# Kernel optimization log

Measured on AMD Instinct MI355X. Metric: run time of the kernel, lower is better.

The kernel has to match this reference:

```python
import jax, jax.numpy as jnp
import numpy as np

N = 20000; E = 320000; F_IN = 128; H = 4; D = 32; HD = 128; G = 8; C = 10


def _ln(x, g, b):
    mu = x.mean(-1, keepdims=True)
    v = ((x - mu) ** 2).mean(-1, keepdims=True)
    return (x - mu) / jnp.sqrt(v + 1e-5) * g + b


def _tconv(x, src, dst, attr, Wq, Wk, Wv, We, Ws, bq, bk, bv, be, bs):
    # PyG TransformerConv (concat=True, beta=False, root_weight=True), eval mode
    n = x.shape[0]
    q = (x @ Wq + bq).reshape(n, H, D)[dst]            # [E,H,D] gather at targets i
    k = (x @ Wk + bk).reshape(n, H, D)[src]            # [E,H,D] gather at sources j
    v = (x @ Wv + bv).reshape(n, H, D)[src]
    ef = (attr @ We + be).reshape(-1, H, D)            # edge features lifted to [E,H,D]
    k = k + ef
    v = v + ef
    logit = (q * k).sum(-1) / jnp.sqrt(jnp.float32(D))  # [E,H]
    m = jax.ops.segment_max(logit, dst, num_segments=n)
    m = jnp.where(jnp.isfinite(m), m, 0.0)
    ex = jnp.exp(logit - m[dst])
    s = jax.ops.segment_sum(ex, dst, num_segments=n)
    alpha = ex / (s[dst] + 1e-16)                      # segment softmax over incoming edges
    out = jax.ops.segment_sum(v * alpha[..., None], dst, num_segments=n).reshape(n, HD)
    out = out + x @ Ws + bs                            # skip / root weight
    return out, alpha


def setup_inputs() -> dict:
    key = jax.random.key(0)
    ks = jax.random.split(key, 50)
    inp = {}
    inp["x"] = jax.random.normal(ks[0], (N, F_IN), jnp.float32)
    inp["edge_index"] = jax.random.randint(ks[1], (2, E), 0, N)
    inp["attr"] = jax.random.normal(ks[2], (E, 1), jnp.float32)
    inp["batch"] = jnp.sort(jax.random.randint(ks[3], (N,), 0, G))
    i = 4
    for l, din in zip((1, 2, 3), (F_IN, HD, HD)):
        for nm, shp in (("Wq", (din, HD)), ("Wk", (din, HD)), ("Wv", (din, HD)), ("We", (1, HD)), ("Ws", (din, HD))):
            inp[f"{nm}{l}"] = jax.random.normal(ks[i], shp, jnp.float32) * 0.05
            i += 1
        for nm in ("bq", "bk", "bv", "be", "bs"):
            inp[f"{nm}{l}"] = jnp.zeros((HD,), jnp.float32)
    inp["ln1_g"] = jnp.ones((HD,), jnp.float32); inp["ln1_b"] = jnp.zeros((HD,), jnp.float32)
    inp["ln2_g"] = jnp.ones((HD,), jnp.float32); inp["ln2_b"] = jnp.zeros((HD,), jnp.float32)
    inp["fc1_w"] = jax.random.normal(ks[i], (HD, HD), jnp.float32) * 0.05; i += 1
    inp["fc1_b"] = jnp.zeros((HD,), jnp.float32)
    inp["cln_g"] = jnp.ones((HD,), jnp.float32); inp["cln_b"] = jnp.zeros((HD,), jnp.float32)
    inp["fc2_w"] = jax.random.normal(ks[i], (HD, C), jnp.float32) * 0.05
    inp["fc2_b"] = jnp.zeros((C,), jnp.float32)
    return inp


def reference(x, edge_index, attr, batch,
              Wq1, Wk1, Wv1, We1, Ws1, bq1, bk1, bv1, be1, bs1,
              Wq2, Wk2, Wv2, We2, Ws2, bq2, bk2, bv2, be2, bs2,
              Wq3, Wk3, Wv3, We3, Ws3, bq3, bk3, bv3, be3, bs3,
              ln1_g, ln1_b, ln2_g, ln2_b,
              fc1_w, fc1_b, cln_g, cln_b, fc2_w, fc2_b):
    src, dst = edge_index[0], edge_index[1]
    h, a1 = _tconv(x, src, dst, attr, Wq1, Wk1, Wv1, We1, Ws1, bq1, bk1, bv1, be1, bs1)
    h = jax.nn.relu(_ln(h, ln1_g, ln1_b))              # dropout is identity in eval
    h, a2 = _tconv(h, src, dst, attr, Wq2, Wk2, Wv2, We2, Ws2, bq2, bk2, bv2, be2, bs2)
    h = jax.nn.relu(_ln(h, ln2_g, ln2_b))
    z, a3 = _tconv(h, src, dst, attr, Wq3, Wk3, Wv3, We3, Ws3, bq3, bk3, bv3, be3, bs3)
    # global mean pool over graphs
    cnt = jax.ops.segment_sum(jnp.ones((N,), z.dtype), batch, num_segments=G)
    z_pool = jax.ops.segment_sum(z, batch, num_segments=G) / jnp.maximum(cnt, 1.0)[:, None]
    # classifier
    hcl = jax.nn.relu(_ln(z_pool @ fc1_w + fc1_b, cln_g, cln_b))
    probs = jax.nn.softmax(hcl @ fc2_w + fc2_b, axis=1)
    z_sel = z_pool[batch[0]]
    return (z, z_sel, probs, a1, a2, a3)
```

## Files before the change

kernel.cpp:

```cpp
#include <hip/hip_runtime.h>


typedef short short8v __attribute__((ext_vector_type(8)));
typedef float f32x4 __attribute__((ext_vector_type(4)));

__device__ __forceinline__ unsigned pack_bf16_rne(float a, float b) {
    unsigned ua = __float_as_uint(a);
    ua += 0x7fffu + ((ua >> 16) & 1u);
    unsigned ub = __float_as_uint(b);
    ub += 0x7fffu + ((ub >> 16) & 1u);
    return (ua >> 16) | (ub & 0xffff0000u);
}

__device__ __forceinline__ unsigned short bf16_rne1(float a) {
    unsigned u = __float_as_uint(a);
    u += 0x7fffu + ((u >> 16) & 1u);
    return (unsigned short)(u >> 16);
}

__global__ __launch_bounds__(256) void hist_kernel(const int* __restrict__ dst,
                                                   int* __restrict__ cnt, int E) {
    int e = blockIdx.x * 256 + threadIdx.x;
    if (e < E) atomicAdd(&cnt[dst[e]], 1);
}

__global__ __launch_bounds__(1024) void scan_kernel(const int* __restrict__ cnt,
                                                    int* __restrict__ rowptr, int n) {
    __shared__ int wls[16];
    __shared__ int carry;
    const int tid = threadIdx.x, lane = tid & 63, wid = tid >> 6;
    if (tid == 0) { carry = 0; rowptr[0] = 0; }
    __syncthreads();
    for (int base = 0; base < n; base += 1024) {
        int i = base + tid;
        int v = (i < n) ? cnt[i] : 0;
        int sc = v;
        for (int off = 1; off < 64; off <<= 1) {
            int t = __shfl_up(sc, off);
            if (lane >= off) sc += t;
        }
        if (lane == 63) wls[wid] = sc;
        __syncthreads();
        if (tid == 0) {
            int run = carry;
            for (int w2 = 0; w2 < 16; ++w2) { int t = wls[w2]; wls[w2] = run; run += t; }
            carry = run;
        }
        __syncthreads();
        if (i < n) rowptr[i + 1] = wls[wid] + sc;
        __syncthreads();
    }
}

__global__ __launch_bounds__(256) void fill_kernel(const int* __restrict__ src,
                                                   const int* __restrict__ dst,
                                                   const float* __restrict__ attr,
                                                   const int* __restrict__ rowptr,
                                                   int* __restrict__ tmp,
                                                   int* __restrict__ src_perm,
                                                   float* __restrict__ attr_perm,
                                                   int* __restrict__ eidp, int E) {
    int e = blockIdx.x * 256 + threadIdx.x;
    if (e < E) {
        int d = dst[e];
        int p = atomicAdd(&tmp[d], 1);
        int pos = rowptr[d] + p;
        src_perm[pos] = src[e];
        attr_perm[pos] = attr[e];
        eidp[pos] = e;
    }
}

__global__ __launch_bounds__(256) void cvt_bf16_kernel(const float* __restrict__ in,
                                                       unsigned* __restrict__ outp, int n32) {
    int i = blockIdx.x * 256 + threadIdx.x;
    if (i < n32) {
        float2 v = *(const float2*)&in[(size_t)i * 2];
        outp[i] = pack_bf16_rne(v.x, v.y);
    }
}

__global__ __launch_bounds__(256) void prepack_kernel(
    const float* __restrict__ W0, const float* __restrict__ W1,
    const float* __restrict__ W2, const float* __restrict__ W3,
    unsigned* __restrict__ wt) {
    const int m = blockIdx.y;
    const float* W = (m == 0) ? W0 : (m == 1) ? W1 : (m == 2) ? W2 : W3;
    int idx = blockIdx.x * 256 + threadIdx.x;
    int c = idx >> 6;
    int kp = idx & 63;
    float w0 = W[(size_t)(2 * kp) * 128 + c];
    float w1 = W[(size_t)(2 * kp + 1) * 128 + c];
    wt[(size_t)m * 8192 + (size_t)c * 64 + kp] = pack_bf16_rne(w0, w1);
}

__global__ __launch_bounds__(256) void gemm_mfma_kernel(
    const unsigned short* __restrict__ Xb, const unsigned short* __restrict__ wt,
    const float* __restrict__ bq, const float* __restrict__ bk,
    const float* __restrict__ bv, const float* __restrict__ bs,
    float* __restrict__ qo, unsigned short* __restrict__ ko,
    unsigned short* __restrict__ vo, float* __restrict__ so, int nrows) {
    const int lane = threadIdx.x & 63;
    const int w = threadIdx.x >> 6;
    const int m = blockIdx.y;
    const int strip = blockIdx.x * 64 + w * 16;
    const int arow = strip + (lane & 15);
    const int arow_c = min(arow, nrows - 1);
    const int kblk = (lane >> 4) * 8;
    const unsigned short* Wm = wt + (size_t)m * 16384;
    const float* bias = (m == 0) ? bq : (m == 1) ? bk : (m == 2) ? bv : bs;

    f32x4 acc[8];
#pragma unroll
    for (int f = 0; f < 8; ++f) acc[f] = (f32x4){0.f, 0.f, 0.f, 0.f};

#pragma unroll
    for (int ks = 0; ks < 4; ++ks) {
        const int k0 = ks * 32 + kblk;
        const short8v a = *(const short8v*)&Xb[(size_t)arow_c * 128 + k0];
#pragma unroll
        for (int f = 0; f < 8; ++f) {
            const short8v b = *(const short8v*)&Wm[(size_t)(f * 16 + (lane & 15)) * 128 + k0];
            acc[f] = __builtin_amdgcn_mfma_f32_16x16x32_bf16(a, b, acc[f], 0, 0, 0);
        }
    }

    const int r0 = strip + (lane >> 4) * 4;
#pragma unroll
    for (int f = 0; f < 8; ++f) {
        const int col = f * 16 + (lane & 15);
        const float bv_ = bias[col];
        if (m == 0 || m == 3) {
            float* OUT = (m == 0) ? qo : so;
#pragma unroll
            for (int r = 0; r < 4; ++r) {
                int row = r0 + r;
                if (row < nrows) OUT[(size_t)row * 128 + col] = acc[f][r] + bv_;
            }
        } else {
            unsigned short* OUT = (m == 1) ? ko : vo;
#pragma unroll
            for (int r = 0; r < 4; ++r) {
                int row = r0 + r;
                if (row < nrows) OUT[(size_t)row * 128 + col] = bf16_rne1(acc[f][r] + bv_);
            }
        }
    }
}

__global__ __launch_bounds__(256) void node_fused_kernel(
    const float* __restrict__ qb, const unsigned* __restrict__ kb,
    const unsigned* __restrict__ vb,
    const float* __restrict__ Wev, const float* __restrict__ bev,
    const int* __restrict__ rowptr, const int* __restrict__ src_perm,
    const float* __restrict__ attr_perm, const int* __restrict__ eidp,
    float* __restrict__ alpha_perm, float* __restrict__ alpha_out,
    float* __restrict__ out, int n) {
    __shared__ float alds[4][64][4];
    const int wid = threadIdx.x >> 6;
    const int node = blockIdx.x * 4 + wid;
    const int lane = threadIdx.x & 63;
    if (node >= n) return;
    const int start = rowptr[node], end = rowptr[node + 1];
    const int deg = end - start;
    if (deg == 0) return;

    const float we0 = Wev[2 * lane], we1 = Wev[2 * lane + 1];
    const float be0 = bev[2 * lane], be1 = bev[2 * lane + 1];
    const float2 qv = *(const float2*)&qb[(size_t)node * 128 + 2 * lane];
    const float scale = 0.17677669529663687f;
    const int h = lane >> 4;

    if (deg <= 64) {
        const bool valid = lane < deg;
        const int j = start + lane;
        const int sj = valid ? src_perm[j] : 0;
        const float aj = valid ? attr_perm[j] : 0.f;

        int t = 0;
        for (; t + 1 < deg; t += 2) {
            const int s0 = __shfl(sj, t), s1 = __shfl(sj, t + 1);
            const float a0 = __shfl(aj, t), a1 = __shfl(aj, t + 1);
            const unsigned u0 = kb[(size_t)s0 * 64 + lane];
            const unsigned u1 = kb[(size_t)s1 * 64 + lane];
            float p0 = qv.x * (__uint_as_float(u0 << 16) + a0 * we0 + be0)
                     + qv.y * (__uint_as_float(u0 & 0xffff0000u) + a0 * we1 + be1);
            float p1 = qv.x * (__uint_as_float(u1 << 16) + a1 * we0 + be0)
                     + qv.y * (__uint_as_float(u1 & 0xffff0000u) + a1 * we1 + be1);
#pragma unroll
            for (int off = 1; off < 16; off <<= 1) {
                p0 += __shfl_xor(p0, off);
                p1 += __shfl_xor(p1, off);
            }
            if ((lane & 15) == 0) {
                alds[wid][t][h] = p0 * scale;
                alds[wid][t + 1][h] = p1 * scale;
            }
        }
        if (t < deg) {
            const int s0 = __shfl(sj, t);
            const float a0 = __shfl(aj, t);
            const unsigned u0 = kb[(size_t)s0 * 64 + lane];
            float p0 = qv.x * (__uint_as_float(u0 << 16) + a0 * we0 + be0)
                     + qv.y * (__uint_as_float(u0 & 0xffff0000u) + a0 * we1 + be1);
#pragma unroll
            for (int off = 1; off < 16; off <<= 1) p0 += __shfl_xor(p0, off);
            if ((lane & 15) == 0) alds[wid][t][h] = p0 * scale;
        }

        float4 lg = valid ? *(const float4*)&alds[wid][lane][0]
                          : make_float4(-1e30f, -1e30f, -1e30f, -1e30f);
        float4 mx = lg;
#pragma unroll
        for (int off = 1; off < 64; off <<= 1) {
            mx.x = fmaxf(mx.x, __shfl_xor(mx.x, off));
            mx.y = fmaxf(mx.y, __shfl_xor(mx.y, off));
            mx.z = fmaxf(mx.z, __shfl_xor(mx.z, off));
            mx.w = fmaxf(mx.w, __shfl_xor(mx.w, off));
        }
        float4 ev;
        ev.x = __expf(lg.x - mx.x); ev.y = __expf(lg.y - mx.y);
        ev.z = __expf(lg.z - mx.z); ev.w = __expf(lg.w - mx.w);
        float4 s4 = ev;
#pragma unroll
        for (int off = 1; off < 64; off <<= 1) {
            s4.x += __shfl_xor(s4.x, off); s4.y += __shfl_xor(s4.y, off);
            s4.z += __shfl_xor(s4.z, off); s4.w += __shfl_xor(s4.w, off);
        }
        float4 al;
        al.x = ev.x / (s4.x + 1e-16f); al.y = ev.y / (s4.y + 1e-16f);
        al.z = ev.z / (s4.z + 1e-16f); al.w = ev.w / (s4.w + 1e-16f);
        if (valid) *(float4*)&alpha_out[(size_t)eidp[j] * 4] = al;
        *(float4*)&alds[wid][lane][0] = al;

        float acc0 = 0.f, acc1 = 0.f;
        t = 0;
        for (; t + 1 < deg; t += 2) {
            const int s0 = __shfl(sj, t), s1 = __shfl(sj, t + 1);
            const float a0 = __shfl(aj, t), a1 = __shfl(aj, t + 1);
            const float w0 = alds[wid][t][h];
            const float w1 = alds[wid][t + 1][h];
            const unsigned u0 = vb[(size_t)s0 * 64 + lane];
            const unsigned u1 = vb[(size_t)s1 * 64 + lane];
            acc0 += w0 * (__uint_as_float(u0 << 16) + a0 * we0 + be0)
                  + w1 * (__uint_as_float(u1 << 16) + a1 * we0 + be0);
            acc1 += w0 * (__uint_as_float(u0 & 0xffff0000u) + a0 * we1 + be1)
                  + w1 * (__uint_as_float(u1 & 0xffff0000u) + a1 * we1 + be1);
        }
        if (t < deg) {
            const int s0 = __shfl(sj, t);
            const float a0 = __shfl(aj, t);
            const float w0 = alds[wid][t][h];
            const unsigned u0 = vb[(size_t)s0 * 64 + lane];
            acc0 += w0 * (__uint_as_float(u0 << 16) + a0 * we0 + be0);
            acc1 += w0 * (__uint_as_float(u0 & 0xffff0000u) + a0 * we1 + be1);
        }
        float2 o = *(float2*)&out[(size_t)node * 128 + 2 * lane];
        o.x += acc0; o.y += acc1;
        *(float2*)&out[(size_t)node * 128 + 2 * lane] = o;
        return;
    }

    float mh = -1e30f;
    for (int c0 = start; c0 < end; c0 += 64) {
        const int nc = min(64, end - c0);
        const int sj = (lane < nc) ? src_perm[c0 + lane] : 0;
        const float aj = (lane < nc) ? attr_perm[c0 + lane] : 0.f;
        int t = 0;
        for (; t + 1 < nc; t += 2) {
            const int s0 = __shfl(sj, t), s1 = __shfl(sj, t + 1);
            const float a0 = __shfl(aj, t), a1 = __shfl(aj, t + 1);
            const unsigned u0 = kb[(size_t)s0 * 64 + lane];
            const unsigned u1 = kb[(size_t)s1 * 64 + lane];
            float p0 = qv.x * (__uint_as_float(u0 << 16) + a0 * we0 + be0)
                     + qv.y * (__uint_as_float(u0 & 0xffff0000u) + a0 * we1 + be1);
            float p1 = qv.x * (__uint_as_float(u1 << 16) + a1 * we0 + be0)
                     + qv.y * (__uint_as_float(u1 & 0xffff0000u) + a1 * we1 + be1);
#pragma unroll
            for (int off = 1; off < 16; off <<= 1) {
                p0 += __shfl_xor(p0, off);
                p1 += __shfl_xor(p1, off);
            }
            p0 *= scale; p1 *= scale;
            mh = fmaxf(mh, fmaxf(p0, p1));
            if ((lane & 15) == 0) {
                alpha_perm[(size_t)(c0 + t) * 4 + h] = p0;
                alpha_perm[(size_t)(c0 + t + 1) * 4 + h] = p1;
            }
        }
        if (t < nc) {
            const int s0 = __shfl(sj, t);
            const float a0 = __shfl(aj, t);
            const unsigned u0 = kb[(size_t)s0 * 64 + lane];
            float p0 = qv.x * (__uint_as_float(u0 << 16) + a0 * we0 + be0)
                     + qv.y * (__uint_as_float(u0 & 0xffff0000u) + a0 * we1 + be1);
#pragma unroll
            for (int off = 1; off < 16; off <<= 1) p0 += __shfl_xor(p0, off);
            p0 *= scale;
            mh = fmaxf(mh, p0);
            if ((lane & 15) == 0) alpha_perm[(size_t)(c0 + t) * 4 + h] = p0;
        }
    }
    const float m0 = __shfl(mh, 0), m1 = __shfl(mh, 16);
    const float m2 = __shfl(mh, 32), m3 = __shfl(mh, 48);

    float4 s4 = make_float4(0.f, 0.f, 0.f, 0.f);
    for (int c0 = start; c0 < end; c0 += 64) {
        const int j = c0 + lane;
        if (j < end) {
            float4 lg = *(const float4*)&alpha_perm[(size_t)j * 4];
            lg.x = __expf(lg.x - m0); lg.y = __expf(lg.y - m1);
            lg.z = __expf(lg.z - m2); lg.w = __expf(lg.w - m3);
            *(float4*)&alpha_perm[(size_t)j * 4] = lg;
            s4.x += lg.x; s4.y += lg.y; s4.z += lg.z; s4.w += lg.w;
        }
    }
#pragma unroll
    for (int off = 1; off < 64; off <<= 1) {
        s4.x += __shfl_xor(s4.x, off); s4.y += __shfl_xor(s4.y, off);
        s4.z += __shfl_xor(s4.z, off); s4.w += __shfl_xor(s4.w, off);
    }
    const float i0 = 1.f / (s4.x + 1e-16f), i1 = 1.f / (s4.y + 1e-16f);
    const float i2 = 1.f / (s4.z + 1e-16f), i3 = 1.f / (s4.w + 1e-16f);

    float acc0 = 0.f, acc1 = 0.f;
    for (int c0 = start; c0 < end; c0 += 64) {
        const int nc = min(64, end - c0);
        const int j = c0 + lane;
        if (lane < nc) {
            float4 ex = *(const float4*)&alpha_perm[(size_t)j * 4];
            float4 al;
            al.x = ex.x * i0; al.y = ex.y * i1; al.z = ex.z * i2; al.w = ex.w * i3;
            *(float4*)&alpha_out[(size_t)eidp[j] * 4] = al;
            *(float4*)&alds[wid][lane][0] = al;
        }
        const int sj = (lane < nc) ? src_perm[j] : 0;
        const float aj = (lane < nc) ? attr_perm[j] : 0.f;
        int t = 0;
        for (; t + 1 < nc; t += 2) {
            const int s0 = __shfl(sj, t), s1 = __shfl(sj, t + 1);
            const float a0 = __shfl(aj, t), a1 = __shfl(aj, t + 1);
            const float w0 = alds[wid][t][h];
            const float w1 = alds[wid][t + 1][h];
            const unsigned u0 = vb[(size_t)s0 * 64 + lane];
            const unsigned u1 = vb[(size_t)s1 * 64 + lane];
            acc0 += w0 * (__uint_as_float(u0 << 16) + a0 * we0 + be0)
                  + w1 * (__uint_as_float(u1 << 16) + a1 * we0 + be0);
            acc1 += w0 * (__uint_as_float(u0 & 0xffff0000u) + a0 * we1 + be1)
                  + w1 * (__uint_as_float(u1 & 0xffff0000u) + a1 * we1 + be1);
        }
        if (t < nc) {
            const int s0 = __shfl(sj, t);
            const float a0 = __shfl(aj, t);
            const float w0 = alds[wid][t][h];
            const unsigned u0 = vb[(size_t)s0 * 64 + lane];
            acc0 += w0 * (__uint_as_float(u0 << 16) + a0 * we0 + be0);
            acc1 += w0 * (__uint_as_float(u0 & 0xffff0000u) + a0 * we1 + be1);
        }
    }
    float2 o = *(float2*)&out[(size_t)node * 128 + 2 * lane];
    o.x += acc0; o.y += acc1;
    *(float2*)&out[(size_t)node * 128 + 2 * lane] = o;
}

__global__ __launch_bounds__(256) void ln_relu_kernel(const float* __restrict__ hin,
                                                      unsigned* __restrict__ hb,
                                                      const float* __restrict__ g,
                                                      const float* __restrict__ b, int n) {
    const int row = (blockIdx.x * 256 + threadIdx.x) >> 6;
    const int lane = threadIdx.x & 63;
    if (row >= n) return;
    const float2 xv = *(const float2*)&hin[(size_t)row * 128 + 2 * lane];
    float s = xv.x + xv.y;
#pragma unroll
    for (int off = 1; off < 64; off <<= 1) s += __shfl_xor(s, off);
    const float mu = s * (1.f / 128.f);
    const float d0 = xv.x - mu, d1 = xv.y - mu;
    float vs = d0 * d0 + d1 * d1;
#pragma unroll
    for (int off = 1; off < 64; off <<= 1) vs += __shfl_xor(vs, off);
    const float inv = rsqrtf(vs * (1.f / 128.f) + 1e-5f);
    const float2 gv = *(const float2*)&g[2 * lane];
    const float2 bv = *(const float2*)&b[2 * lane];
    const float n0 = fmaxf(d0 * inv * gv.x + bv.x, 0.f);
    const float n1 = fmaxf(d1 * inv * gv.y + bv.y, 0.f);
    hb[(size_t)row * 64 + lane] = pack_bf16_rne(n0, n1);
}

__global__ __launch_bounds__(128) void pool_kernel(const float* __restrict__ z,
                                                   const int* __restrict__ batch,
                                                   float* __restrict__ pool,
                                                   int* __restrict__ gcnt, int n) {
    const int c = threadIdx.x;
    const int row0 = blockIdx.x * 32;
    if (row0 >= n) return;
    const int rend = min(row0 + 32, n);
    int cur = batch[row0];
    float acc = 0.f;
    int run = 0;
    for (int r = row0; r < rend; ++r) {
        const int g = batch[r];
        if (g != cur) {
            atomicAdd(&pool[cur * 128 + c], acc);
            if (c == 0) atomicAdd(&gcnt[cur], run);
            acc = 0.f; run = 0; cur = g;
        }
        acc += z[(size_t)r * 128 + c];
        ++run;
    }
    atomicAdd(&pool[cur * 128 + c], acc);
    if (c == 0) atomicAdd(&gcnt[cur], run);
}

__global__ __launch_bounds__(128) void classifier_kernel(
    const float* __restrict__ pool, const int* __restrict__ gcnt,
    const int* __restrict__ batch,
    const float* __restrict__ fc1_w, const float* __restrict__ fc1_b,
    const float* __restrict__ cg, const float* __restrict__ cbv,
    const float* __restrict__ fc2_w, const float* __restrict__ fc2_b,
    float* __restrict__ zsel, float* __restrict__ probs) {
    __shared__ float zp[8][128];
    __shared__ float hc[8][128];
    __shared__ float red[2];
    __shared__ float lgt[8][10];
    const int c = threadIdx.x;
    const int lane = c & 63, wid = c >> 6;
#pragma unroll
    for (int g = 0; g < 8; ++g)
        zp[g][c] = pool[g * 128 + c] / fmaxf((float)gcnt[g], 1.f);
    __syncthreads();
    zsel[c] = zp[batch[0]][c];

    float acc[8];
#pragma unroll
    for (int g = 0; g < 8; ++g) acc[g] = fc1_b[c];
    for (int k = 0; k < 128; ++k) {
        const float w = fc1_w[k * 128 + c];
#pragma unroll
        for (int g = 0; g < 8; ++g) acc[g] += zp[g][k] * w;
    }
#pragma unroll
    for (int g = 0; g < 8; ++g) {
        float s = acc[g];
        for (int off = 1; off < 64; off <<= 1) s += __shfl_xor(s, off);
        if (lane == 0) red[wid] = s;
        __syncthreads();
        const float mu = (red[0] + red[1]) * (1.f / 128.f);
        __syncthreads();
        const float d = acc[g] - mu;
        float s2 = d * d;
        for (int off = 1; off < 64; off <<= 1) s2 += __shfl_xor(s2, off);
        if (lane == 0) red[wid] = s2;
        __syncthreads();
        const float var = (red[0] + red[1]) * (1.f / 128.f);
        __syncthreads();
        hc[g][c] = fmaxf(d * rsqrtf(var + 1e-5f) * cg[c] + cbv[c], 0.f);
    }
    __syncthreads();
    if (c < 80) {
        const int g = c / 10, j = c - g * 10;
        float s = fc2_b[j];
        for (int k = 0; k < 128; ++k) s += hc[g][k] * fc2_w[k * 10 + j];
        lgt[g][j] = s;
    }
    __syncthreads();
    if (c < 8) {
        float mx = -1e30f;
#pragma unroll
        for (int j = 0; j < 10; ++j) mx = fmaxf(mx, lgt[c][j]);
        float ex[10];
        float sum = 0.f;
#pragma unroll
        for (int j = 0; j < 10; ++j) { ex[j] = expf(lgt[c][j] - mx); sum += ex[j]; }
#pragma unroll
        for (int j = 0; j < 10; ++j) probs[c * 10 + j] = ex[j] / sum;
    }
}


extern "C" void kernel_launch(void* const* d_in, const int* in_sizes, int n_in,
                              void* d_out, int out_size, void* d_ws, size_t ws_size,
                              hipStream_t stream) {
    const float* x = (const float*)d_in[0];
    const int* edge_index = (const int*)d_in[1];
    const float* attr = (const float*)d_in[2];
    const int* batch = (const int*)d_in[3];
    const int N = in_sizes[0] / 128;
    const int E = in_sizes[2];
    const int* src = edge_index;
    const int* dst = edge_index + E;

    const float *Wq[3], *Wk[3], *Wv[3], *We[3], *Ws[3];
    const float *bq[3], *bk[3], *bv[3], *be[3], *bs[3];
    int idx = 4;
    for (int l = 0; l < 3; ++l) {
        Wq[l] = (const float*)d_in[idx++];
        Wk[l] = (const float*)d_in[idx++];
        Wv[l] = (const float*)d_in[idx++];
        We[l] = (const float*)d_in[idx++];
        Ws[l] = (const float*)d_in[idx++];
        bq[l] = (const float*)d_in[idx++];
        bk[l] = (const float*)d_in[idx++];
        bv[l] = (const float*)d_in[idx++];
        be[l] = (const float*)d_in[idx++];
        bs[l] = (const float*)d_in[idx++];
    }
    const float* ln_g[2] = {(const float*)d_in[34], (const float*)d_in[36]};
    const float* ln_b[2] = {(const float*)d_in[35], (const float*)d_in[37]};
    const float* fc1_w = (const float*)d_in[38];
    const float* fc1_b = (const float*)d_in[39];
    const float* cln_g = (const float*)d_in[40];
    const float* cln_b = (const float*)d_in[41];
    const float* fc2_w = (const float*)d_in[42];
    const float* fc2_b = (const float*)d_in[43];
    const int C = in_sizes[43];

    float* out = (float*)d_out;
    float* z_out = out;
    float* zsel_out = out + (size_t)N * 128;
    float* probs_out = zsel_out + 128;
    const int GC = out_size - N * 128 - 128 - 3 * E * 4;
    const int G = GC / C;
    float* alpha_out[3];
    alpha_out[0] = probs_out + GC;
    alpha_out[1] = alpha_out[0] + (size_t)E * 4;
    alpha_out[2] = alpha_out[1] + (size_t)E * 4;

    char* p = (char*)d_ws;
    auto alloc = [&](size_t bytes) {
        void* r = (void*)p;
        p += (bytes + 255) & ~(size_t)255;
        return r;
    };
    float* qb = (float*)alloc((size_t)N * 128 * 4);
    unsigned* kb = (unsigned*)alloc((size_t)N * 64 * 4);
    unsigned* vb = (unsigned*)alloc((size_t)N * 64 * 4);
    float* hA = (float*)alloc((size_t)N * 128 * 4);
    float* hB = (float*)alloc((size_t)N * 128 * 4);
    unsigned* xb = (unsigned*)alloc((size_t)N * 64 * 4);
    unsigned* hb = (unsigned*)alloc((size_t)N * 64 * 4);
    unsigned* wt = (unsigned*)alloc((size_t)12 * 8192 * 4);
    int* counts = (int*)alloc((size_t)N * 4);
    int* rowptr = (int*)alloc((size_t)(N + 1) * 4);
    int* cnt2 = (int*)alloc((size_t)N * 4);
    int* src_perm = (int*)alloc((size_t)E * 4);
    float* attr_perm = (float*)alloc((size_t)E * 4);
    int* eidp = (int*)alloc((size_t)E * 4);
    float* alpha_perm = (float*)alloc((size_t)E * 4 * 4);
    float* pool = (float*)alloc((size_t)G * 128 * 4);
    int* gcnt = (int*)alloc((size_t)G * 4);

    hipMemsetAsync(counts, 0, (size_t)N * 4, stream);
    hipMemsetAsync(cnt2, 0, (size_t)N * 4, stream);
    hipMemsetAsync(pool, 0, (size_t)G * 128 * 4, stream);
    hipMemsetAsync(gcnt, 0, (size_t)G * 4, stream);

    hist_kernel<<<(E + 255) / 256, 256, 0, stream>>>(dst, counts, E);
    scan_kernel<<<1, 1024, 0, stream>>>(counts, rowptr, N);
    fill_kernel<<<(E + 255) / 256, 256, 0, stream>>>(src, dst, attr, rowptr, cnt2,
                                                     src_perm, attr_perm, eidp, E);

    cvt_bf16_kernel<<<(N * 64 + 255) / 256, 256, 0, stream>>>(x, xb, N * 64);
    for (int l = 0; l < 3; ++l)
        prepack_kernel<<<dim3(32, 4), 256, 0, stream>>>(Wq[l], Wk[l], Wv[l], Ws[l],
                                                        wt + (size_t)l * 4 * 8192);

    for (int l = 0; l < 3; ++l) {
        float* OUTl = (l == 0) ? hA : (l == 1) ? hB : z_out;
        const unsigned short* Xin = (const unsigned short*)((l == 0) ? xb : hb);
        gemm_mfma_kernel<<<dim3((N + 63) / 64, 4), 256, 0, stream>>>(
            Xin, (const unsigned short*)(wt + (size_t)l * 4 * 8192),
            bq[l], bk[l], bv[l], bs[l],
            qb, (unsigned short*)kb, (unsigned short*)vb, OUTl, N);
        node_fused_kernel<<<(N + 3) / 4, 256, 0, stream>>>(
            qb, kb, vb, We[l], be[l], rowptr, src_perm, attr_perm, eidp,
            alpha_perm, alpha_out[l], OUTl, N);
        if (l < 2)
            ln_relu_kernel<<<((N + 3) / 4), 256, 0, stream>>>(OUTl, hb, ln_g[l], ln_b[l], N);
    }

    pool_kernel<<<(N + 31) / 32, 128, 0, stream>>>(z_out, batch, pool, gcnt, N);
    classifier_kernel<<<1, 128, 0, stream>>>(pool, gcnt, batch, fc1_w, fc1_b,
                                             cln_g, cln_b, fc2_w, fc2_b,
                                             zsel_out, probs_out);
}
```

Before: 523.9 us.

## Fuse LayerNorm+ReLU into node kernel, parallelize CSR scan, hoist edge-feature algebra

Folds the LayerNorm+ReLU epilogue into the per-node attention kernel, so the intermediate hidden state is never written and reread, which also removes two launches. The edge-feature terms are hoisted algebraically: q·we and q·be are reduced once per node, and the attention-weighted attr sum is applied once at the end. Both gather loops are unrolled by four for more memory-level parallelism. The single-block serial scan becomes a three-kernel parallel scan, and the three weight-prepack launches are merged into one. Costs are more register pressure in the fused kernel and slightly different float rounding order.

```diff
diff --git a/kernel.cpp b/kernel.cpp
--- a/kernel.cpp
+++ b/kernel.cpp
@@ -18,38 +18,67 @@
     return (unsigned short)(u >> 16);
 }
 
+__device__ __forceinline__ float blo(unsigned u) { return __uint_as_float(u << 16); }
+__device__ __forceinline__ float bhi(unsigned u) { return __uint_as_float(u & 0xffff0000u); }
+
 __global__ __launch_bounds__(256) void hist_kernel(const int* __restrict__ dst,
                                                    int* __restrict__ cnt, int E) {
     int e = blockIdx.x * 256 + threadIdx.x;
     if (e < E) atomicAdd(&cnt[dst[e]], 1);
 }
 
-__global__ __launch_bounds__(1024) void scan_kernel(const int* __restrict__ cnt,
-                                                    int* __restrict__ rowptr, int n) {
+__global__ __launch_bounds__(256) void blk_reduce_kernel(const int* __restrict__ cnt,
+                                                         int* __restrict__ bsum, int n) {
+    __shared__ int ws[4];
+    const int i = blockIdx.x * 256 + threadIdx.x;
+    const int lane = threadIdx.x & 63, wid = threadIdx.x >> 6;
+    int v = (i < n) ? cnt[i] : 0;
+#pragma unroll
+    for (int off = 1; off < 64; off <<= 1) v += __shfl_xor(v, off);
+    if (lane == 0) ws[wid] = v;
+    __syncthreads();
+    if (threadIdx.x == 0) bsum[blockIdx.x] = ws[0] + ws[1] + ws[2] + ws[3];
+}
+
+__global__ __launch_bounds__(1024) void blk_scan_kernel(int* __restrict__ bsum, int nb) {
     __shared__ int wls[16];
-    __shared__ int carry;
     const int tid = threadIdx.x, lane = tid & 63, wid = tid >> 6;
-    if (tid == 0) { carry = 0; rowptr[0] = 0; }
+    int v = (tid < nb) ? bsum[tid] : 0;
+    int sc = v;
+#pragma unroll
+    for (int off = 1; off < 64; off <<= 1) {
+        int t = __shfl_up(sc, off);
+        if (lane >= off) sc += t;
+    }
+    if (lane == 63) wls[wid] = sc;
     __syncthreads();
-    for (int base = 0; base < n; base += 1024) {
-        int i = base + tid;
-        int v = (i < n) ? cnt[i] : 0;
-        int sc = v;
-        for (int off = 1; off < 64; off <<= 1) {
-            int t = __shfl_up(sc, off);
-            if (lane >= off) sc += t;
-        }
-        if (lane == 63) wls[wid] = sc;
-        __syncthreads();
-        if (tid == 0) {
-            int run = carry;
-            for (int w2 = 0; w2 < 16; ++w2) { int t = wls[w2]; wls[w2] = run; run += t; }
-            carry = run;
-        }
-        __syncthreads();
-        if (i < n) rowptr[i + 1] = wls[wid] + sc;
-        __syncthreads();
-    }
+    if (tid == 0) {
+        int run = 0;
+        for (int w = 0; w < 16; ++w) { int t = wls[w]; wls[w] = run; run += t; }
+    }
+    __syncthreads();
+    if (tid < nb) bsum[tid] = wls[wid] + sc - v;
+}
+
+__global__ __launch_bounds__(256) void rowptr_fill_kernel(const int* __restrict__ cnt,
+                                                          const int* __restrict__ boff,
+                                                          int* __restrict__ rowptr, int n) {
+    __shared__ int wls[4];
+    const int i = blockIdx.x * 256 + threadIdx.x;
+    const int lane = threadIdx.x & 63, wid = threadIdx.x >> 6;
+    int v = (i < n) ? cnt[i] : 0;
+    int sc = v;
+#pragma unroll
+    for (int off = 1; off < 64; off <<= 1) {
+        int t = __shfl_up(sc, off);
+        if (lane >= off) sc += t;
+    }
+    if (lane == 63) wls[wid] = sc;
+    __syncthreads();
+    int add = boff[blockIdx.x];
+    for (int w = 0; w < wid; ++w) add += wls[w];
+    if (i < n) rowptr[i + 1] = sc + add;
+    if (i == 0) rowptr[0] = 0;
 }
 
 __global__ __launch_bounds__(256) void fill_kernel(const int* __restrict__ src,
@@ -80,18 +109,15 @@
     }
 }
 
-__global__ __launch_bounds__(256) void prepack_kernel(
-    const float* __restrict__ W0, const float* __restrict__ W1,
-    const float* __restrict__ W2, const float* __restrict__ W3,
-    unsigned* __restrict__ wt) {
+struct W12 { const float* p[12]; };
+__global__ __launch_bounds__(256) void prepack_all_kernel(W12 ws, unsigned* __restrict__ wt) {
     const int m = blockIdx.y;
-    const float* W = (m == 0) ? W0 : (m == 1) ? W1 : (m == 2) ? W2 : W3;
+    const float* W = ws.p[m];
     int idx = blockIdx.x * 256 + threadIdx.x;
     int c = idx >> 6;
     int kp = idx & 63;
-    float w0 = W[(size_t)(2 * kp) * 128 + c];
-    float w1 = W[(size_t)(2 * kp + 1) * 128 + c];
-    wt[(size_t)m * 8192 + (size_t)c * 64 + kp] = pack_bf16_rne(w0, w1);
+    wt[(size_t)m * 8192 + (size_t)c * 64 + kp] =
+        pack_bf16_rne(W[(size_t)(2 * kp) * 128 + c], W[(size_t)(2 * kp + 1) * 128 + c]);
 }
 
 __global__ __launch_bounds__(256) void gemm_mfma_kernel(
@@ -155,7 +181,10 @@
     const int* __restrict__ rowptr, const int* __restrict__ src_perm,
     const float* __restrict__ attr_perm, const int* __restrict__ eidp,
     float* __restrict__ alpha_perm, float* __restrict__ alpha_out,
-    float* __restrict__ out, int n) {
+    const float* __restrict__ skip, float* __restrict__ zout,
+    unsigned* __restrict__ hbout,
+    const float* __restrict__ lng, const float* __restrict__ lnb,
+    int do_ln, int n) {
     __shared__ float alds[4][64][4];
     const int wid = threadIdx.x >> 6;
     const int node = blockIdx.x * 4 + wid;
@@ -163,49 +192,63 @@
     if (node >= n) return;
     const int start = rowptr[node], end = rowptr[node + 1];
     const int deg = end - start;
-    if (deg == 0) return;
-
+    const int h = lane >> 4;
     const float we0 = Wev[2 * lane], we1 = Wev[2 * lane + 1];
     const float be0 = bev[2 * lane], be1 = bev[2 * lane + 1];
     const float2 qv = *(const float2*)&qb[(size_t)node * 128 + 2 * lane];
     const float scale = 0.17677669529663687f;
-    const int h = lane >> 4;
-
-    if (deg <= 64) {
+    const bool fastp = (deg <= 64);
+
+    float acc0 = 0.f, acc1 = 0.f, sa = 0.f;
+
+    if (deg > 0 && fastp) {
+        float pw = qv.x * we0 + qv.y * we1;
+        float pb = qv.x * be0 + qv.y * be1;
+#pragma unroll
+        for (int off = 1; off < 16; off <<= 1) {
+            pw += __shfl_xor(pw, off);
+            pb += __shfl_xor(pb, off);
+        }
+
         const bool valid = lane < deg;
         const int j = start + lane;
         const int sj = valid ? src_perm[j] : 0;
         const float aj = valid ? attr_perm[j] : 0.f;
 
         int t = 0;
-        for (; t + 1 < deg; t += 2) {
+        for (; t + 3 < deg; t += 4) {
             const int s0 = __shfl(sj, t), s1 = __shfl(sj, t + 1);
+            const int s2 = __shfl(sj, t + 2), s3 = __shfl(sj, t + 3);
             const float a0 = __shfl(aj, t), a1 = __shfl(aj, t + 1);
+            const float a2 = __shfl(aj, t + 2), a3 = __shfl(aj, t + 3);
             const unsigned u0 = kb[(size_t)s0 * 64 + lane];
             const unsigned u1 = kb[(size_t)s1 * 64 + lane];
-            float p0 = qv.x * (__uint_as_float(u0 << 16) + a0 * we0 + be0)
-                     + qv.y * (__uint_as_float(u0 & 0xffff0000u) + a0 * we1 + be1);
-            float p1 = qv.x * (__uint_as_float(u1 << 16) + a1 * we0 + be0)
-                     + qv.y * (__uint_as_float(u1 & 0xffff0000u) + a1 * we1 + be1);
+            const unsigned u2 = kb[(size_t)s2 * 64 + lane];
+            const unsigned u3 = kb[(size_t)s3 * 64 + lane];
+            float p0 = qv.x * blo(u0) + qv.y * bhi(u0);
+            float p1 = qv.x * blo(u1) + qv.y * bhi(u1);
+            float p2 = qv.x * blo(u2) + qv.y * bhi(u2);
+            float p3 = qv.x * blo(u3) + qv.y * bhi(u3);
 #pragma unroll
             for (int off = 1; off < 16; off <<= 1) {
-                p0 += __shfl_xor(p0, off);
-                p1 += __shfl_xor(p1, off);
+                p0 += __shfl_xor(p0, off); p1 += __shfl_xor(p1, off);
+                p2 += __shfl_xor(p2, off); p3 += __shfl_xor(p3, off);
             }
             if ((lane & 15) == 0) {
-                alds[wid][t][h] = p0 * scale;
-                alds[wid][t + 1][h] = p1 * scale;
-            }
-        }
-        if (t < deg) {
+                alds[wid][t + 0][h] = (p0 + a0 * pw + pb) * scale;
+                alds[wid][t + 1][h] = (p1 + a1 * pw + pb) * scale;
+                alds[wid][t + 2][h] = (p2 + a2 * pw + pb) * scale;
+                alds[wid][t + 3][h] = (p3 + a3 * pw + pb) * scale;
+            }
+        }
+        for (; t < deg; ++t) {
             const int s0 = __shfl(sj, t);
             const float a0 = __shfl(aj, t);
             const unsigned u0 = kb[(size_t)s0 * 64 + lane];
-            float p0 = qv.x * (__uint_as_float(u0 << 16) + a0 * we0 + be0)
-                     + qv.y * (__uint_as_float(u0 & 0xffff0000u) + a0 * we1 + be1);
+            float p0 = qv.x * blo(u0) + qv.y * bhi(u0);
 #pragma unroll
             for (int off = 1; off < 16; off <<= 1) p0 += __shfl_xor(p0, off);
-            if ((lane & 15) == 0) alds[wid][t][h] = p0 * scale;
+            if ((lane & 15) == 0) alds[wid][t][h] = (p0 + a0 * pw + pb) * scale;
         }
 
         float4 lg = valid ? *(const float4*)&alds[wid][lane][0]
@@ -233,158 +276,155 @@
         if (valid) *(float4*)&alpha_out[(size_t)eidp[j] * 4] = al;
         *(float4*)&alds[wid][lane][0] = al;
 
-        float acc0 = 0.f, acc1 = 0.f;
         t = 0;
-        for (; t + 1 < deg; t += 2) {
+        for (; t + 3 < deg; t += 4) {
             const int s0 = __shfl(sj, t), s1 = __shfl(sj, t + 1);
+            const int s2 = __shfl(sj, t + 2), s3 = __shfl(sj, t + 3);
             const float a0 = __shfl(aj, t), a1 = __shfl(aj, t + 1);
-            const float w0 = alds[wid][t][h];
+            const float a2 = __shfl(aj, t + 2), a3 = __shfl(aj, t + 3);
+            const float w0 = alds[wid][t + 0][h];
             const float w1 = alds[wid][t + 1][h];
+            const float w2 = alds[wid][t + 2][h];
+            const float w3 = alds[wid][t + 3][h];
             const unsigned u0 = vb[(size_t)s0 * 64 + lane];
             const unsigned u1 = vb[(size_t)s1 * 64 + lane];
-            acc0 += w0 * (__uint_as_float(u0 << 16) + a0 * we0 + be0)
-                  + w1 * (__uint_as_float(u1 << 16) + a1 * we0 + be0);
-            acc1 += w0 * (__uint_as_float(u0 & 0xffff0000u) + a0 * we1 + be1)
-                  + w1 * (__uint_as_float(u1 & 0xffff0000u) + a1 * we1 + be1);
-        }
-        if (t < deg) {
+            const unsigned u2 = vb[(size_t)s2 * 64 + lane];
+            const unsigned u3 = vb[(size_t)s3 * 64 + lane];
+            acc0 += w0 * blo(u0) + w1 * blo(u1) + w2 * blo(u2) + w3 * blo(u3);
+            acc1 += w0 * bhi(u0) + w1 * bhi(u1) + w2 * bhi(u2) + w3 * bhi(u3);
+            sa += w0 * a0 + w1 * a1 + w2 * a2 + w3 * a3;
+        }
+        for (; t < deg; ++t) {
             const int s0 = __shfl(sj, t);
             const float a0 = __shfl(aj, t);
             const float w0 = alds[wid][t][h];
             const unsigned u0 = vb[(size_t)s0 * 64 + lane];
-            acc0 += w0 * (__uint_as_float(u0 << 16) + a0 * we0 + be0);
-            acc1 += w0 * (__uint_as_float(u0 & 0xffff0000u) + a0 * we1 + be1);
-        }
-        float2 o = *(float2*)&out[(size_t)node * 128 + 2 * lane];
-        o.x += acc0; o.y += acc1;
-        *(float2*)&out[(size_t)node * 128 + 2 * lane] = o;
-        return;
-    }
-
-    float mh = -1e30f;
-    for (int c0 = start; c0 < end; c0 += 64) {
-        const int nc = min(64, end - c0);
-        const int sj = (lane < nc) ? src_perm[c0 + lane] : 0;
-        const float aj = (lane < nc) ? attr_perm[c0 + lane] : 0.f;
-        int t = 0;
-        for (; t + 1 < nc; t += 2) {
-            const int s0 = __shfl(sj, t), s1 = __shfl(sj, t + 1);
-            const float a0 = __shfl(aj, t), a1 = __shfl(aj, t + 1);
-            const unsigned u0 = kb[(size_t)s0 * 64 + lane];
-            const unsigned u1 = kb[(size_t)s1 * 64 + lane];
-            float p0 = qv.x * (__uint_as_float(u0 << 16) + a0 * we0 + be0)
-                     + qv.y * (__uint_as_float(u0 & 0xffff0000u) + a0 * we1 + be1);
-            float p1 = qv.x * (__uint_as_float(u1 << 16) + a1 * we0 + be0)
-                     + qv.y * (__uint_as_float(u1 & 0xffff0000u) + a1 * we1 + be1);
-#pragma unroll
-            for (int off = 1; off < 16; off <<= 1) {
-                p0 += __shfl_xor(p0, off);
-                p1 += __shfl_xor(p1, off);
-            }
-            p0 *= scale; p1 *= scale;
-            mh = fmaxf(mh, fmaxf(p0, p1));
-            if ((lane & 15) == 0) {
-                alpha_perm[(size_t)(c0 + t) * 4 + h] = p0;
-                alpha_perm[(size_t)(c0 + t + 1) * 4 + h] = p1;
-            }
-        }
-        if (t < nc) {
-            const int s0 = __shfl(sj, t);
-            const float a0 = __shfl(aj, t);
-            const unsigned u0 = kb[(size_t)s0 * 64 + lane];
-            float p0 = qv.x * (__uint_as_float(u0 << 16) + a0 * we0 + be0)
-                     + qv.y * (__uint_as_float(u0 & 0xffff0000u) + a0 * we1 + be1);
-#pragma unroll
-            for (int off = 1; off < 16; off <<= 1) p0 += __shfl_xor(p0, off);
-            p0 *= scale;
-            mh = fmaxf(mh, p0);
-            if ((lane & 15) == 0) alpha_perm[(size_t)(c0 + t) * 4 + h] = p0;
-        }
-    }
-    const float m0 = __shfl(mh, 0), m1 = __shfl(mh, 16);
-    const float m2 = __shfl(mh, 32), m3 = __shfl(mh, 48);
-
-    float4 s4 = make_float4(0.f, 0.f, 0.f, 0.f);
-    for (int c0 = start; c0 < end; c0 += 64) {
-        const int j = c0 + lane;
-        if (j < end) {
-            float4 lg = *(const float4*)&alpha_perm[(size_t)j * 4];
-            lg.x = __expf(lg.x - m0); lg.y = __expf(lg.y - m1);
-            lg.z = __expf(lg.z - m2); lg.w = __expf(lg.w - m3);
-            *(float4*)&alpha_perm[(size_t)j * 4] = lg;
-            s4.x += lg.x; s4.y += lg.y; s4.z += lg.z; s4.w += lg.w;
-        }
-    }
-#pragma unroll
-    for (int off = 1; off < 64; off <<= 1) {
-        s4.x += __shfl_xor(s4.x, off); s4.y += __shfl_xor(s4.y, off);
-        s4.z += __shfl_xor(s4.z, off); s4.w += __shfl_xor(s4.w, off);
-    }
-    const float i0 = 1.f / (s4.x + 1e-16f), i1 = 1.f / (s4.y + 1e-16f);
-    const float i2 = 1.f / (s4.z + 1e-16f), i3 = 1.f / (s4.w + 1e-16f);
-
-    float acc0 = 0.f, acc1 = 0.f;
-    for (int c0 = start; c0 < end; c0 += 64) {
-        const int nc = min(64, end - c0);
-        const int j = c0 + lane;
-        if (lane < nc) {
-            float4 ex = *(const float4*)&alpha_perm[(size_t)j * 4];
-            float4 al;
-            al.x = ex.x * i0; al.y = ex.y * i1; al.z = ex.z * i2; al.w = ex.w * i3;
-            *(float4*)&alpha_out[(size_t)eidp[j] * 4] = al;
-            *(float4*)&alds[wid][lane][0] = al;
-        }
-        const int sj = (lane < nc) ? src_perm[j] : 0;
-        const float aj = (lane < nc) ? attr_perm[j] : 0.f;
-        int t = 0;
-        for (; t + 1 < nc; t += 2) {
-            const int s0 = __shfl(sj, t), s1 = __shfl(sj, t + 1);
-            const float a0 = __shfl(aj, t), a1 = __shfl(aj, t + 1);
-            const float w0 = alds[wid][t][h];
-            const float w1 = alds[wid][t + 1][h];
-            const unsigned u0 = vb[(size_t)s0 * 64 + lane];
-            const unsigned u1 = vb[(size_t)s1 * 64 + lane];
-            acc0 += w0 * (__uint_as_float(u0 << 16) + a0 * we0 + be0)
-                  + w1 * (__uint_as_float(u1 << 16) + a1 * we0 + be0);
-            acc1 += w0 * (__uint_as_float(u0 & 0xffff0000u) + a0 * we1 + be1)
-                  + w1 * (__uint_as_float(u1 & 0xffff0000u) + a1 * we1 + be1);
-        }
-        if (t < nc) {
-            const int s0 = __shfl(sj, t);
-            const float a0 = __shfl(aj, t);
-            const float w0 = alds[wid][t][h];
-            const unsigned u0 = vb[(size_t)s0 * 64 + lane];
-            acc0 += w0 * (__uint_as_float(u0 << 16) + a0 * we0 + be0);
-            acc1 += w0 * (__uint_as_float(u0 & 0xffff0000u) + a0 * we1 + be1);
-        }
-    }
-    float2 o = *(float2*)&out[(size_t)node * 128 + 2 * lane];
-    o.x += acc0; o.y += acc1;
-    *(float2*)&out[(size_t)node * 128 + 2 * lane] = o;
-}
-
-__global__ __launch_bounds__(256) void ln_relu_kernel(const float* __restrict__ hin,
-                                                      unsigned* __restrict__ hb,
-                                                      const float* __restrict__ g,
-                                                      const float* __restrict__ b, int n) {
-    const int row = (blockIdx.x * 256 + threadIdx.x) >> 6;
-    const int lane = threadIdx.x & 63;
-    if (row >= n) return;
-    const float2 xv = *(const float2*)&hin[(size_t)row * 128 + 2 * lane];
-    float s = xv.x + xv.y;
-#pragma unroll
-    for (int off = 1; off < 64; off <<= 1) s += __shfl_xor(s, off);
-    const float mu = s * (1.f / 128.f);
-    const float d0 = xv.x - mu, d1 = xv.y - mu;
-    float vs = d0 * d0 + d1 * d1;
-#pragma unroll
-    for (int off = 1; off < 64; off <<= 1) vs += __shfl_xor(vs, off);
-    const float inv = rsqrtf(vs * (1.f / 128.f) + 1e-5f);
-    const float2 gv = *(const float2*)&g[2 * lane];
-    const float2 bv = *(const float2*)&b[2 * lane];
-    const float n0 = fmaxf(d0 * inv * gv.x + bv.x, 0.f);
-    const float n1 = fmaxf(d1 * inv * gv.y + bv.y, 0.f);
-    hb[(size_t)row * 64 + lane] = pack_bf16_rne(n0, n1);
+            acc0 += w0 * blo(u0);
+            acc1 += w0 * bhi(u0);
+            sa += w0 * a0;
+        }
+    } else if (deg > 0) {
+        float mh = -1e30f;
+        for (int c0 = start; c0 < end; c0 += 64) {
+            const int nc = min(64, end - c0);
+            const int sj = (lane < nc) ? src_perm[c0 + lane] : 0;
+            const float aj = (lane < nc) ? attr_perm[c0 + lane] : 0.f;
+            int t = 0;
+            for (; t + 1 < nc; t += 2) {
+                const int s0 = __shfl(sj, t), s1 = __shfl(sj, t + 1);
+                const float a0 = __shfl(aj, t), a1 = __shfl(aj, t + 1);
+                const unsigned u0 = kb[(size_t)s0 * 64 + lane];
+                const unsigned u1 = kb[(size_t)s1 * 64 + lane];
+                float p0 = qv.x * (blo(u0) + a0 * we0 + be0) + qv.y * (bhi(u0) + a0 * we1 + be1);
+                float p1 = qv.x * (blo(u1) + a1 * we0 + be0) + qv.y * (bhi(u1) + a1 * we1 + be1);
+#pragma unroll
+                for (int off = 1; off < 16; off <<= 1) {
+                    p0 += __shfl_xor(p0, off);
+                    p1 += __shfl_xor(p1, off);
+                }
+                p0 *= scale; p1 *= scale;
+                mh = fmaxf(mh, fmaxf(p0, p1));
+                if ((lane & 15) == 0) {
+                    alpha_perm[(size_t)(c0 + t) * 4 + h] = p0;
+                    alpha_perm[(size_t)(c0 + t + 1) * 4 + h] = p1;
+                }
+            }
+            if (t < nc) {
+                const int s0 = __shfl(sj, t);
+                const float a0 = __shfl(aj, t);
+                const unsigned u0 = kb[(size_t)s0 * 64 + lane];
+                float p0 = qv.x * (blo(u0) + a0 * we0 + be0) + qv.y * (bhi(u0) + a0 * we1 + be1);
+#pragma unroll
+                for (int off = 1; off < 16; off <<= 1) p0 += __shfl_xor(p0, off);
+                p0 *= scale;
+                mh = fmaxf(mh, p0);
+                if ((lane & 15) == 0) alpha_perm[(size_t)(c0 + t) * 4 + h] = p0;
+            }
+        }
+        const float m0 = __shfl(mh, 0), m1 = __shfl(mh, 16);
+        const float m2 = __shfl(mh, 32), m3 = __shfl(mh, 48);
+
+        float4 s4 = make_float4(0.f, 0.f, 0.f, 0.f);
+        for (int c0 = start; c0 < end; c0 += 64) {
+            const int j = c0 + lane;
+            if (j < end) {
+                float4 lg = *(const float4*)&alpha_perm[(size_t)j * 4];
+                lg.x = __expf(lg.x - m0); lg.y = __expf(lg.y - m1);
+                lg.z = __expf(lg.z - m2); lg.w = __expf(lg.w - m3);
+                *(float4*)&alpha_perm[(size_t)j * 4] = lg;
+                s4.x += lg.x; s4.y += lg.y; s4.z += lg.z; s4.w += lg.w;
+            }
+        }
+#pragma unroll
+        for (int off = 1; off < 64; off <<= 1) {
+            s4.x += __shfl_xor(s4.x, off); s4.y += __shfl_xor(s4.y, off);
+            s4.z += __shfl_xor(s4.z, off); s4.w += __shfl_xor(s4.w, off);
+        }
+        const float i0 = 1.f / (s4.x + 1e-16f), i1 = 1.f / (s4.y + 1e-16f);
+        const float i2 = 1.f / (s4.z + 1e-16f), i3 = 1.f / (s4.w + 1e-16f);
+
+        for (int c0 = start; c0 < end; c0 += 64) {
+            const int nc = min(64, end - c0);
+            const int j = c0 + lane;
+            if (lane < nc) {
+                float4 ex = *(const float4*)&alpha_perm[(size_t)j * 4];
+                float4 al;
+                al.x = ex.x * i0; al.y = ex.y * i1; al.z = ex.z * i2; al.w = ex.w * i3;
+                *(float4*)&alpha_out[(size_t)eidp[j] * 4] = al;
+                *(float4*)&alds[wid][lane][0] = al;
+            }
+            const int sj = (lane < nc) ? src_perm[j] : 0;
+            const float aj = (lane < nc) ? attr_perm[j] : 0.f;
+            int t = 0;
+            for (; t + 1 < nc; t += 2) {
+                const int s0 = __shfl(sj, t), s1 = __shfl(sj, t + 1);
+                const float a0 = __shfl(aj, t), a1 = __shfl(aj, t + 1);
+                const float w0 = alds[wid][t][h];
+                const float w1 = alds[wid][t + 1][h];
+                const unsigned u0 = vb[(size_t)s0 * 64 + lane];
+                const unsigned u1 = vb[(size_t)s1 * 64 + lane];
+                acc0 += w0 * (blo(u0) + a0 * we0 + be0) + w1 * (blo(u1) + a1 * we0 + be0);
+                acc1 += w0 * (bhi(u0) + a0 * we1 + be1) + w1 * (bhi(u1) + a1 * we1 + be1);
+            }
+            if (t < nc) {
+                const int s0 = __shfl(sj, t);
+                const float a0 = __shfl(aj, t);
+                const float w0 = alds[wid][t][h];
+                const unsigned u0 = vb[(size_t)s0 * 64 + lane];
+                acc0 += w0 * (blo(u0) + a0 * we0 + be0);
+                acc1 += w0 * (bhi(u0) + a0 * we1 + be1);
+            }
+        }
+    }
+
+    float2 o = *(const float2*)&skip[(size_t)node * 128 + 2 * lane];
+    if (deg > 0) {
+        if (fastp) {
+            o.x += acc0 + sa * we0 + be0;
+            o.y += acc1 + sa * we1 + be1;
+        } else {
+            o.x += acc0;
+            o.y += acc1;
+        }
+    }
+    if (do_ln) {
+        float s = o.x + o.y;
+#pragma unroll
+        for (int off = 1; off < 64; off <<= 1) s += __shfl_xor(s, off);
+        const float mu = s * (1.f / 128.f);
+        const float d0 = o.x - mu, d1 = o.y - mu;
+        float vs = d0 * d0 + d1 * d1;
+#pragma unroll
+        for (int off = 1; off < 64; off <<= 1) vs += __shfl_xor(vs, off);
+        const float inv = rsqrtf(vs * (1.f / 128.f) + 1e-5f);
+        const float2 gv = *(const float2*)&lng[2 * lane];
+        const float2 bv2 = *(const float2*)&lnb[2 * lane];
+        const float n0 = fmaxf(d0 * inv * gv.x + bv2.x, 0.f);
+        const float n1 = fmaxf(d1 * inv * gv.y + bv2.y, 0.f);
+        hbout[(size_t)node * 64 + lane] = pack_bf16_rne(n0, n1);
+    } else {
+        *(float2*)&zout[(size_t)node * 128 + 2 * lane] = o;
+    }
 }
 
 __global__ __launch_bounds__(128) void pool_kernel(const float* __restrict__ z,
@@ -536,13 +576,13 @@
     unsigned* kb = (unsigned*)alloc((size_t)N * 64 * 4);
     unsigned* vb = (unsigned*)alloc((size_t)N * 64 * 4);
     float* hA = (float*)alloc((size_t)N * 128 * 4);
-    float* hB = (float*)alloc((size_t)N * 128 * 4);
     unsigned* xb = (unsigned*)alloc((size_t)N * 64 * 4);
     unsigned* hb = (unsigned*)alloc((size_t)N * 64 * 4);
     unsigned* wt = (unsigned*)alloc((size_t)12 * 8192 * 4);
     int* counts = (int*)alloc((size_t)N * 4);
     int* rowptr = (int*)alloc((size_t)(N + 1) * 4);
     int* cnt2 = (int*)alloc((size_t)N * 4);
+    int* bsum = (int*)alloc((size_t)1024 * 4);
     int* src_perm = (int*)alloc((size_t)E * 4);
     float* attr_perm = (float*)alloc((size_t)E * 4);
     int* eidp = (int*)alloc((size_t)E * 4);
@@ -555,28 +595,34 @@
     hipMemsetAsync(pool, 0, (size_t)G * 128 * 4, stream);
     hipMemsetAsync(gcnt, 0, (size_t)G * 4, stream);
 
+    const int nb = (N + 255) / 256;
     hist_kernel<<<(E + 255) / 256, 256, 0, stream>>>(dst, counts, E);
-    scan_kernel<<<1, 1024, 0, stream>>>(counts, rowptr, N);
+    blk_reduce_kernel<<<nb, 256, 0, stream>>>(counts, bsum, N);
+    blk_scan_kernel<<<1, 1024, 0, stream>>>(bsum, nb);
+    rowptr_fill_kernel<<<nb, 256, 0, stream>>>(counts, bsum, rowptr, N);
     fill_kernel<<<(E + 255) / 256, 256, 0, stream>>>(src, dst, attr, rowptr, cnt2,
                                                      src_perm, attr_perm, eidp, E);
 
     cvt_bf16_kernel<<<(N * 64 + 255) / 256, 256, 0, stream>>>(x, xb, N * 64);
-    for (int l = 0; l < 3; ++l)
-        prepack_kernel<<<dim3(32, 4), 256, 0, stream>>>(Wq[l], Wk[l], Wv[l], Ws[l],
-                                                        wt + (size_t)l * 4 * 8192);
-
+    W12 ws;
     for (int l = 0; l < 3; ++l) {
-        float* OUTl = (l == 0) ? hA : (l == 1) ? hB : z_out;
+        ws.p[l * 4 + 0] = Wq[l]; ws.p[l * 4 + 1] = Wk[l];
+        ws.p[l * 4 + 2] = Wv[l]; ws.p[l * 4 + 3] = Ws[l];
+    }
+    prepack_all_kernel<<<dim3(32, 12), 256, 0, stream>>>(ws, wt);
+
+    for (int l = 0; l < 3; ++l) {
+        float* SKIP = (l < 2) ? hA : z_out;
         const unsigned short* Xin = (const unsigned short*)((l == 0) ? xb : hb);
         gemm_mfma_kernel<<<dim3((N + 63) / 64, 4), 256, 0, stream>>>(
             Xin, (const unsigned short*)(wt + (size_t)l * 4 * 8192),
             bq[l], bk[l], bv[l], bs[l],
-            qb, (unsigned short*)kb, (unsigned short*)vb, OUTl, N);
+            qb, (unsigned short*)kb, (unsigned short*)vb, SKIP, N);
         node_fused_kernel<<<(N + 3) / 4, 256, 0, stream>>>(
             qb, kb, vb, We[l], be[l], rowptr, src_perm, attr_perm, eidp,
-            alpha_perm, alpha_out[l], OUTl, N);
-        if (l < 2)
-            ln_relu_kernel<<<((N + 3) / 4), 256, 0, stream>>>(OUTl, hb, ln_g[l], ln_b[l], N);
+            alpha_perm, alpha_out[l], SKIP, z_out, hb,
+            (l < 2) ? ln_g[l] : ln_g[0], (l < 2) ? ln_b[l] : ln_b[0],
+            (l < 2) ? 1 : 0, N);
     }
 
     pool_kernel<<<(N + 31) / 32, 128, 0, stream>>>(z_out, batch, pool, gcnt, N);
```

Result: faster. 501.8 us (-4.2%).
